# Performance work log

Hardware: AMD Instinct MI355X
Metric: run time of the kernel (lower is better)

The kernel has to match this reference:

```python
import jax, jax.numpy as jnp
import numpy as np

POOL_H, POOL_W = 7, 7
SPATIAL_SCALE = 0.25
SAMPLING_RATIO = 2
ALIGNED = True


def setup_inputs() -> dict:
    key = jax.random.key(0)
    k1, k2, k3, k4, k5 = jax.random.split(key, 5)
    N, C, H, W = 4, 256, 200, 200
    K = 1024
    feat = jax.random.normal(k1, (N, C, H, W), dtype=jnp.float32)
    # boxes in image coordinates (image side = H / spatial_scale = 800)
    img = H / SPATIAL_SCALE
    b = jax.random.randint(k2, (K,), 0, N).astype(jnp.float32)
    x1 = jax.random.uniform(k3, (K,)) * (img - 32.0)
    y1 = jax.random.uniform(k4, (K,)) * (img - 32.0)
    wh = jax.random.uniform(k5, (K, 2)) * 256.0 + 16.0
    x2 = jnp.minimum(x1 + wh[:, 0], img - 1.0)
    y2 = jnp.minimum(y1 + wh[:, 1], img - 1.0)
    rois = jnp.stack([b, x1, y1, x2, y2], axis=1)
    return {"input": feat, "rois": rois}


def _roi_align(feat, rois):
    N, C, H, W = feat.shape
    K = rois.shape[0]
    S = SAMPLING_RATIO
    offset = 0.5 if ALIGNED else 0.0

    batch_idx = rois[:, 0].astype(jnp.int32)
    x1 = rois[:, 1] * SPATIAL_SCALE - offset
    y1 = rois[:, 2] * SPATIAL_SCALE - offset
    x2 = rois[:, 3] * SPATIAL_SCALE - offset
    y2 = rois[:, 4] * SPATIAL_SCALE - offset
    roi_w = x2 - x1
    roi_h = y2 - y1
    if not ALIGNED:  # legacy: clamp roi size to at least 1
        roi_w = jnp.maximum(roi_w, 1.0)
        roi_h = jnp.maximum(roi_h, 1.0)
    bin_h = roi_h / POOL_H  # [K]
    bin_w = roi_w / POOL_W

    # sample coordinates: ys [K, PH, S], xs [K, PW, S]
    ph = jnp.arange(POOL_H, dtype=jnp.float32)
    pw = jnp.arange(POOL_W, dtype=jnp.float32)
    s = (jnp.arange(S, dtype=jnp.float32) + 0.5) / S
    ys = y1[:, None, None] + (ph[None, :, None] + s[None, None, :]) * bin_h[:, None, None]
    xs = x1[:, None, None] + (pw[None, :, None] + s[None, None, :]) * bin_w[:, None, None]

    # broadcast to full sample grid [K, PH, S, PW, S]
    y = ys[:, :, :, None, None]
    x = xs[:, None, None, :, :]
    valid = (y > -1.0) & (y < H) & (x > -1.0) & (x < W)

    yc = jnp.clip(y, 0.0, H - 1)
    xc = jnp.clip(x, 0.0, W - 1)
    y0 = jnp.floor(yc).astype(jnp.int32)
    x0 = jnp.floor(xc).astype(jnp.int32)
    y1i = jnp.minimum(y0 + 1, H - 1)
    x1i = jnp.minimum(x0 + 1, W - 1)
    ly = yc - y0
    lx = xc - x0
    hy = 1.0 - ly
    hx = 1.0 - lx

    bi = batch_idx[:, None, None, None, None]
    # advanced indexing -> [K, PH, S, PW, S, C]
    v00 = feat[bi, :, y0, x0]
    v01 = feat[bi, :, y0, x1i]
    v10 = feat[bi, :, y1i, x0]
    v11 = feat[bi, :, y1i, x1i]

    val = ((hy * hx)[..., None] * v00 + (hy * lx)[..., None] * v01
           + (ly * hx)[..., None] * v10 + (ly * lx)[..., None] * v11)
    val = jnp.where(valid[..., None], val, 0.0)

    out = val.sum(axis=(2, 4)) / (S * S)  # [K, PH, PW, C]
    return jnp.transpose(out, (0, 3, 1, 2))  # [K, C, PH, PW]


def reference(input, rois):
    return _roi_align(input, rois)
```

## Files before the change

### kernel.cpp

```cpp
#include <hip/hip_runtime.h>

#define POOL_H 7
#define POOL_W 7
#define BINS   49
#define SR 2
#define SCALE 0.25f
#define CH 256

typedef unsigned int   u32;
typedef unsigned short u16;
typedef unsigned long long u64;
typedef float f2v __attribute__((ext_vector_type(2)));
typedef f2v uf2 __attribute__((aligned(4)));
typedef float f4  __attribute__((ext_vector_type(4)));
typedef u32  ui4 __attribute__((ext_vector_type(4)));

__device__ __forceinline__ u16 f32_to_bf16_rne(float f) {
    u32 u = __builtin_bit_cast(u32, f);
    u32 r = (u + 0x7FFFu + ((u >> 16) & 1u)) >> 16;
    return (u16)r;
}
__device__ __forceinline__ float bf16lo(u32 u) { return __builtin_bit_cast(float, u << 16); }
__device__ __forceinline__ float bf16hi(u32 u) { return __builtin_bit_cast(float, u & 0xFFFF0000u); }

__device__ __forceinline__ void gload_lds16(const float* g, float* l) {
    __builtin_amdgcn_global_load_lds(
        (const __attribute__((address_space(1))) void*)g,
        (__attribute__((address_space(3))) void*)l,
        16, 0, 0);
}

__global__ __launch_bounds__(512) void nchw_to_nhwc_bf16(
    const float* __restrict__ feat, u16* __restrict__ ft,
    const float* __restrict__ rois, int* __restrict__ perm,
    int HW, int tiles, int K, int H, int W)
{
    __shared__ __align__(16) unsigned char smem[32768];

    int t = threadIdx.x;

    if ((int)blockIdx.x == gridDim.x - 1) {
        u64* keys = (u64*)smem;
        int bd = (int)blockDim.x;
        for (int v = t; v < 1024; v += bd) {
            u64 kv = ~0ull;
            if (v < K) {
                const float* rp = rois + (size_t)v * 5;
                int b = (int)rp[0];
                float cx = 0.5f * (rp[1] + rp[3]) * SCALE;
                float cy = 0.5f * (rp[2] + rp[4]) * SCALE;
                int qx = min(15, max(0, (int)(cx * (16.0f / (float)W))));
                int qy = min(15, max(0, (int)(cy * (16.0f / (float)H))));
                u32 m = 0;
                #pragma unroll
                for (int i = 0; i < 4; ++i)
                    m |= (((qy >> i) & 1u) << (2 * i + 1)) | (((qx >> i) & 1u) << (2 * i));
                u32 key = ((u32)b << 8) | m;
                kv = ((u64)key << 32) | (u32)v;
            }
            keys[v] = kv;
        }
        __syncthreads();
        for (int size = 2; size <= 1024; size <<= 1) {
            for (int stride = size >> 1; stride > 0; stride >>= 1) {
                for (int v = t; v < 1024; v += bd) {
                    int j = v ^ stride;
                    if (j > v) {
                        bool up = ((v & size) == 0);
                        u64 a = keys[v], bb = keys[j];
                        if ((a > bb) == up) { keys[v] = bb; keys[j] = a; }
                    }
                }
                __syncthreads();
            }
        }
        for (int v = t; v < K; v += bd)
            perm[v] = (int)(keys[v] & 0xffffffffu);
        return;
    }

    float* lf = (float*)smem;
    int bid   = blockIdx.x;
    int chalf = bid & 1;
    int tile  = (bid >> 1) % tiles;
    int b     = (bid >> 1) / tiles;
    int hw0   = tile * 64;

    int lane = t & 63;
    int w    = t >> 6;

    const float* src = feat + ((size_t)b * CH + (size_t)chalf * 128) * HW + hw0;
    #pragma unroll
    for (int ii = 0; ii < 4; ++ii) {
        int i = w * 4 + ii;
        int r = 4 * i + (lane >> 4);
        int hwb = (4 * (lane & 15) - 4 * (r >> 3)) & 63;
        gload_lds16(src + (size_t)r * HW + hwb, &lf[i * 256]);
    }
    __syncthreads();

    u16* dst = ft + ((size_t)b * HW + hw0) * CH + chalf * 128;
    #pragma unroll
    for (int it = 0; it < 2; ++it) {
        int cg = t & 15;
        int hw = it * 32 + (t >> 4);
        int q  = (hw + 4 * cg) & 63;
        u32 o[4];
        #pragma unroll
        for (int d = 0; d < 4; ++d) {
            int c0 = 8 * cg + 2 * d;
            float va = lf[(size_t)c0 * 64 + q];
            float vb = lf[(size_t)(c0 + 1) * 64 + q];
            o[d] = ((u32)f32_to_bf16_rne(vb) << 16) | (u32)f32_to_bf16_rne(va);
        }
        *(ui4*)(dst + (size_t)hw * CH + 8 * cg) = *(ui4*)o;
    }
}

__global__ __launch_bounds__(448) void roi_gather_nhwc(
    const u16* __restrict__ ft,
    const float* __restrict__ rois,
    const int* __restrict__ perm,
    float* __restrict__ out,
    int H, int W, int K, int chunk, int do_swz)
{
    int bid  = blockIdx.x;
    int slot = do_swz ? (bid & 7) * chunk + (bid >> 3) : bid;
    int k    = perm[slot / 7];
    int q    = slot % 7;
    int bin0 = q * 7;

    __shared__ float lds[7][CH];

    int lane = threadIdx.x & 63;
    int w    = threadIdx.x >> 6;
    int half = lane >> 5;
    int lc   = lane & 31;

    const float* rp = rois + (size_t)k * 5;
    int   b   = (int)rp[0];
    float rx1 = rp[1] * SCALE - 0.5f;
    float ry1 = rp[2] * SCALE - 0.5f;
    float rx2 = rp[3] * SCALE - 0.5f;
    float ry2 = rp[4] * SCALE - 0.5f;
    float bin_h = (ry2 - ry1) * (1.0f / POOL_H);
    float bin_w = (rx2 - rx1) * (1.0f / POOL_W);

    const u16* fbase = ft + (size_t)b * H * W * CH + lc * 8;

    int ph = q;
    int pw = w;

    float acc[8];
    #pragma unroll
    for (int j = 0; j < 8; ++j) acc[j] = 0.0f;

    #pragma unroll
    for (int iy = 0; iy < SR; ++iy) {
        float y = ry1 + ((float)ph + ((float)iy + 0.5f) * (1.0f / SR)) * bin_h;
        bool vy = (y > -1.0f) && (y < (float)H);
        float yc = fminf(fmaxf(y, 0.0f), (float)(H - 1));
        int   y0 = (int)yc;
        int   y1 = min(y0 + 1, H - 1);
        float ly = yc - (float)y0;
        float hy = 1.0f - ly;
        int   ysel = half ? y1 : y0;
        float wrow = half ? ly : hy;
        #pragma unroll
        for (int ix = 0; ix < SR; ++ix) {
            float x = rx1 + ((float)pw + ((float)ix + 0.5f) * (1.0f / SR)) * bin_w;
            bool vx = (x > -1.0f) && (x < (float)W);
            if (!(vy && vx)) continue;
            float xc = fminf(fmaxf(x, 0.0f), (float)(W - 1));
            int   x0 = (int)xc;
            int   x1 = min(x0 + 1, W - 1);
            float lx = xc - (float)x0;

            const u16* p0 = fbase + (size_t)(ysel * W + x0) * CH;
            ui4 A = *(const ui4*)p0;
            ui4 B = *(const ui4*)(p0 + (size_t)(x1 - x0) * CH);

            #pragma unroll
            for (int j = 0; j < 4; ++j) {
                float a0 = bf16lo(A[j]), a1 = bf16hi(A[j]);
                float b0 = bf16lo(B[j]), b1 = bf16hi(B[j]);
                float r0 = a0 + lx * (b0 - a0);
                float r1 = a1 + lx * (b1 - a1);
                acc[2 * j]     += wrow * r0;
                acc[2 * j + 1] += wrow * r1;
            }
        }
    }

    #pragma unroll
    for (int j = 0; j < 8; ++j)
        acc[j] = (acc[j] + __shfl_xor(acc[j], 32, 64)) * 0.25f;

    if (half == 0) {
        f4 lo = { acc[0], acc[1], acc[2], acc[3] };
        f4 hi = { acc[4], acc[5], acc[6], acc[7] };
        *(f4*)&lds[w][lc * 8]     = lo;
        *(f4*)&lds[w][lc * 8 + 4] = hi;
    }
    __syncthreads();

    float* ob = out + (size_t)k * CH * BINS + bin0;
    for (int id = (int)threadIdx.x; id < 7 * CH; id += 448) {
        int c  = id / 7;
        int lb = id % 7;
        ob[(size_t)c * BINS + lb] = lds[lb][c];
    }
}

#define NC 2
#define NXCD 8
__global__ __launch_bounds__(256) void roi_align_fallback(
    const float* __restrict__ feat, const float* __restrict__ rois,
    float* __restrict__ out, int C, int H, int W, int K,
    int blocks_per_slice, int slices_per_xcd)
{
    int wgid  = blockIdx.x;
    int g     = wgid % NXCD;
    int r     = wgid / NXCD;
    int slice = g * slices_per_xcd + r / blocks_per_slice;
    int j     = r % blocks_per_slice;
    int tid = j * (int)blockDim.x + (int)threadIdx.x;
    int k   = tid / BINS;
    int bin = tid % BINS;
    if (k >= K) return;
    int pw = bin % POOL_W, ph = bin / POOL_W, c2 = slice;

    const float* rp = rois + (size_t)k * 5;
    int b = (int)rp[0];
    float rx1 = rp[1]*SCALE-0.5f, ry1 = rp[2]*SCALE-0.5f;
    float rx2 = rp[3]*SCALE-0.5f, ry2 = rp[4]*SCALE-0.5f;
    float bin_h = (ry2-ry1)*(1.0f/POOL_H), bin_w = (rx2-rx1)*(1.0f/POOL_W);

    int yr0[SR], yr1[SR]; float ly[SR], hy[SR]; bool vy[SR];
    #pragma unroll
    for (int iy = 0; iy < SR; ++iy) {
        float y = ry1 + ((float)ph + ((float)iy+0.5f)*(1.0f/SR))*bin_h;
        vy[iy] = (y > -1.0f) && (y < (float)H);
        float yc = fminf(fmaxf(y, 0.0f), (float)(H-1));
        int y0 = (int)yc; yr0[iy]=y0; yr1[iy]=min(y0+1,H-1);
        ly[iy]=yc-(float)y0; hy[iy]=1.0f-ly[iy];
    }
    int xl[SR]; float lx[SR]; bool vx[SR], xhi[SR];
    #pragma unroll
    for (int ix = 0; ix < SR; ++ix) {
        float x = rx1 + ((float)pw + ((float)ix+0.5f)*(1.0f/SR))*bin_w;
        vx[ix] = (x > -1.0f) && (x < (float)W);
        float xc = fminf(fmaxf(x, 0.0f), (float)(W-1));
        int x0 = (int)xc; int xload = min(x0, W-2);
        xl[ix]=xload; xhi[ix]=(x0>xload); lx[ix]=xc-(float)x0;
    }
    const size_t HW = (size_t)H*W;
    const float* fmap = feat + ((size_t)b*C + (size_t)c2*NC)*HW;
    float acc[NC];
    #pragma unroll
    for (int cc=0; cc<NC; ++cc) acc[cc]=0.0f;
    #pragma unroll
    for (int iy=0; iy<SR; ++iy)
      #pragma unroll
      for (int ix=0; ix<SR; ++ix)
        if (vy[iy] && vx[ix]) {
            int off0 = yr0[iy]*W + xl[ix], off1 = yr1[iy]*W + xl[ix];
            #pragma unroll
            for (int cc=0; cc<NC; ++cc) {
                const float* base = fmap + (size_t)cc*HW;
                f2v d0 = *(const uf2*)(base + off0);
                f2v d1 = *(const uf2*)(base + off1);
                float v00 = xhi[ix] ? d0.y : d0.x;
                float v10 = xhi[ix] ? d1.y : d1.x;
                float r0 = v00 + lx[ix]*(d0.y - v00);
                float r1 = v10 + lx[ix]*(d1.y - v10);
                acc[cc] += hy[iy]*r0 + ly[iy]*r1;
            }
        }
    size_t obase = ((size_t)k*C + (size_t)c2*NC)*BINS + bin;
    #pragma unroll
    for (int cc=0; cc<NC; ++cc)
        out[obase + (size_t)cc*BINS] = acc[cc]*(1.0f/(SR*SR));
}

extern "C" void kernel_launch(void* const* d_in, const int* in_sizes, int n_in,
                              void* d_out, int out_size, void* d_ws, size_t ws_size,
                              hipStream_t stream) {
    const float* feat = (const float*)d_in[0];
    const float* rois = (const float*)d_in[1];
    float* out = (float*)d_out;

    const int C = 256, H = 200, W = 200;
    const int HW = H * W;
    const int K = in_sizes[1] / 5;
    const int N = in_sizes[0] / (C * HW);

    size_t nhwc_bytes = (size_t)N * HW * CH * sizeof(u16);
    size_t need = nhwc_bytes + (size_t)K * sizeof(int);
    if (ws_size >= need && (HW % 64) == 0 && K <= 1024) {
        u16* ft   = (u16*)d_ws;
        int* perm = (int*)((char*)d_ws + nhwc_bytes);
        const int tiles = HW / 64;
        nchw_to_nhwc_bf16<<<N * tiles * 2 + 1, 512, 0, stream>>>(
            feat, ft, rois, perm, HW, tiles, K, H, W);
        int grid  = K * 7;
        int swz   = (grid % 8) == 0;
        int chunk = grid / 8;
        roi_gather_nhwc<<<grid, 448, 0, stream>>>(
            (const u16*)ft, rois, perm, out, H, W, K, chunk, swz);
    } else {
        const int threads_per_slice = K * BINS;
        const int block = 256;
        const int blocks_per_slice = (threads_per_slice + block - 1) / block;
        const int slices = C / NC;
        const int slices_per_xcd = slices / NXCD;
        const int grid = slices * blocks_per_slice;
        roi_align_fallback<<<grid, block, 0, stream>>>(feat, rois, out, C, H, W, K,
                                                       blocks_per_slice, slices_per_xcd);
    }
}
```

Before: 96.72 us.

## Retile NCHW-to-NHWC bf16 transpose into 64-channel by 512-pixel windows

Rewrites the layout-conversion kernel so each block handles 64 channels by 512 spatial positions instead of 128 channels by 64 positions. Data is loaded directly into registers as float4, converted to packed bf16 before the LDS store, and written to a rotated, padded LDS layout to avoid bank conflicts. The direct-to-LDS global load path is removed. The intent is longer contiguous global reads, half the LDS footprint per element, and fewer blocks, at the cost of higher register pressure from 16 float4 values per thread and more bit extraction in the store phase.

```diff
diff --git a/kernel.cpp b/kernel.cpp
--- a/kernel.cpp
+++ b/kernel.cpp
@@ -23,24 +23,16 @@
 __device__ __forceinline__ float bf16lo(u32 u) { return __builtin_bit_cast(float, u << 16); }
 __device__ __forceinline__ float bf16hi(u32 u) { return __builtin_bit_cast(float, u & 0xFFFF0000u); }
 
-__device__ __forceinline__ void gload_lds16(const float* g, float* l) {
-    __builtin_amdgcn_global_load_lds(
-        (const __attribute__((address_space(1))) void*)g,
-        (__attribute__((address_space(3))) void*)l,
-        16, 0, 0);
-}
-
 __global__ __launch_bounds__(512) void nchw_to_nhwc_bf16(
     const float* __restrict__ feat, u16* __restrict__ ft,
     const float* __restrict__ rois, int* __restrict__ perm,
-    int HW, int tiles, int K, int H, int W)
+    int HW, int nwin, int K, int H, int W, int N)
 {
-    __shared__ __align__(16) unsigned char smem[32768];
-
+    __shared__ u32 lds32[64 * 258];
     int t = threadIdx.x;
 
     if ((int)blockIdx.x == gridDim.x - 1) {
-        u64* keys = (u64*)smem;
+        __shared__ u64 keys[1024];
         int bd = (int)blockDim.x;
         for (int v = t; v < 1024; v += bd) {
             u64 kv = ~0ull;
@@ -79,41 +71,57 @@
         return;
     }
 
-    float* lf = (float*)smem;
-    int bid   = blockIdx.x;
-    int chalf = bid & 1;
-    int tile  = (bid >> 1) % tiles;
-    int b     = (bid >> 1) / tiles;
-    int hw0   = tile * 64;
-
-    int lane = t & 63;
-    int w    = t >> 6;
-
-    const float* src = feat + ((size_t)b * CH + (size_t)chalf * 128) * HW + hw0;
-    #pragma unroll
-    for (int ii = 0; ii < 4; ++ii) {
-        int i = w * 4 + ii;
-        int r = 4 * i + (lane >> 4);
-        int hwb = (4 * (lane & 15) - 4 * (r >> 3)) & 63;
-        gload_lds16(src + (size_t)r * HW + hwb, &lf[i * 256]);
+    int bid = blockIdx.x;
+    int win = bid / (4 * N);
+    int rr  = bid % (4 * N);
+    int ct  = rr / N;
+    int b   = rr % N;
+    int hw0 = win * 512;
+    int nhw = min(512, HW - hw0);
+
+    int row = t >> 3;
+    int seg = t & 7;
+
+    const float* src = feat + ((size_t)b * CH + (size_t)ct * 64 + row) * HW + hw0;
+
+    f4 v[16];
+    #pragma unroll
+    for (int m = 0; m < 16; ++m) {
+        int chunk = m * 8 + seg;
+        if (chunk * 4 < nhw) v[m] = *(const f4*)(src + chunk * 4);
+        else                 v[m] = (f4){0.f, 0.f, 0.f, 0.f};
+    }
+    #pragma unroll
+    for (int m = 0; m < 16; ++m) {
+        int chunk = m * 8 + seg;
+        u32 p0 = ((u32)f32_to_bf16_rne(v[m].y) << 16) | (u32)f32_to_bf16_rne(v[m].x);
+        u32 p1 = ((u32)f32_to_bf16_rne(v[m].w) << 16) | (u32)f32_to_bf16_rne(v[m].z);
+        int hp = chunk * 2;
+        lds32[row * 258 + ((hp     + row) & 255)] = p0;
+        lds32[row * 258 + ((hp + 1 + row) & 255)] = p1;
     }
     __syncthreads();
 
-    u16* dst = ft + ((size_t)b * HW + hw0) * CH + chalf * 128;
-    #pragma unroll
-    for (int it = 0; it < 2; ++it) {
-        int cg = t & 15;
-        int hw = it * 32 + (t >> 4);
-        int q  = (hw + 4 * cg) & 63;
-        u32 o[4];
-        #pragma unroll
-        for (int d = 0; d < 4; ++d) {
-            int c0 = 8 * cg + 2 * d;
-            float va = lf[(size_t)c0 * 64 + q];
-            float vb = lf[(size_t)(c0 + 1) * 64 + q];
-            o[d] = ((u32)f32_to_bf16_rne(vb) << 16) | (u32)f32_to_bf16_rne(va);
-        }
-        *(ui4*)(dst + (size_t)hw * CH + 8 * cg) = *(ui4*)o;
+    u16* dst = ft + ((size_t)b * HW + hw0) * CH + ct * 64;
+    int j   = t & 7;
+    int hwo = t >> 3;
+    #pragma unroll
+    for (int i = 0; i < 8; ++i) {
+        int hw = i * 64 + hwo;
+        if (hw < nhw) {
+            int hp = hw >> 1, half = hw & 1;
+            u32 o[4];
+            #pragma unroll
+            for (int d = 0; d < 4; ++d) {
+                int c0 = j * 8 + 2 * d;
+                u32 a  = lds32[c0       * 258 + ((hp + c0)     & 255)];
+                u32 bb = lds32[(c0 + 1) * 258 + ((hp + c0 + 1) & 255)];
+                u32 lo = half ? (a  >> 16) : (a  & 0xFFFFu);
+                u32 hi = half ? (bb >> 16) : (bb & 0xFFFFu);
+                o[d] = (hi << 16) | lo;
+            }
+            *(ui4*)(dst + (size_t)hw * CH + j * 8) = *(ui4*)o;
+        }
     }
 }
 
@@ -297,12 +305,12 @@
 
     size_t nhwc_bytes = (size_t)N * HW * CH * sizeof(u16);
     size_t need = nhwc_bytes + (size_t)K * sizeof(int);
-    if (ws_size >= need && (HW % 64) == 0 && K <= 1024) {
+    if (ws_size >= need && K <= 1024) {
         u16* ft   = (u16*)d_ws;
         int* perm = (int*)((char*)d_ws + nhwc_bytes);
-        const int tiles = HW / 64;
-        nchw_to_nhwc_bf16<<<N * tiles * 2 + 1, 512, 0, stream>>>(
-            feat, ft, rois, perm, HW, tiles, K, H, W);
+        const int nwin = (HW + 511) / 512;
+        nchw_to_nhwc_bf16<<<nwin * 4 * N + 1, 512, 0, stream>>>(
+            feat, ft, rois, perm, HW, nwin, K, H, W, N);
         int grid  = K * 7;
         int swz   = (grid % 8) == 0;
         int chunk = grid / 8;
```

Result: faster. 94.56 us (-2.2%).
